# Optimization experiments

Measured on AMD Instinct MI355X. Metric: run time of the kernel, lower is better.

Reference implementation:

```python
import jax, jax.numpy as jnp
import numpy as np

N_ATOMS = 50000
N_PAIRS = 800000
X_DIM = 3
N_PROP = 64


def setup_inputs() -> dict:
    key = jax.random.key(0)
    k1, k2, k3, k4 = jax.random.split(key, 4)
    ind_2 = jax.random.randint(k1, (N_PAIRS, 2), 0, N_ATOMS, dtype=jnp.int64 if jax.config.jax_enable_x64 else jnp.int32)
    px = jax.random.normal(k2, (N_ATOMS, X_DIM, N_PROP), dtype=jnp.float32)
    wi = jax.random.normal(k3, (N_PROP, N_PROP), dtype=jnp.float32) / np.sqrt(N_PROP)
    wj = jax.random.normal(k4, (N_PROP, N_PROP), dtype=jnp.float32) / np.sqrt(N_PROP)
    return {"ind_2": ind_2, "px": px, "wi": wi, "wj": wj}


def reference(ind_2, px, wi, wj):
    # gather node equivariant props per edge endpoint
    px_i = px[ind_2[:, 0]]  # (n_pairs, x, n_prop)
    px_j = px[ind_2[:, 1]]  # (n_pairs, x, n_prop)
    # weighted branch: Dense(no bias) on last dim for each endpoint, then sum
    return jnp.einsum("pxz,zg->pxg", px_i, wi) + jnp.einsum("pxz,zg->pxg", px_j, wj)
```

## Files before the change

kernel.cpp:

```cpp
#include <hip/hip_runtime.h>

#define NPROP 64

typedef float vf4 __attribute__((ext_vector_type(4)));

__global__ __launch_bounds__(64, 2)
void transform_kernel(const float* __restrict__ px,
                      const float* __restrict__ wi,
                      const float* __restrict__ wj,
                      float* __restrict__ A,
                      float* __restrict__ B,
                      int nrows) {
    const int g = threadIdx.x;

    float WA[NPROP], WB[NPROP];
#pragma unroll
    for (int z = 0; z < NPROP; ++z) {
        WA[z] = wi[z * NPROP + g];
        WB[z] = wj[z * NPROP + g];
    }

    for (int r = blockIdx.x; r < nrows; r += gridDim.x) {
        const float* __restrict__ row = px + (size_t)r * NPROP;
        float a = 0.0f, b = 0.0f;
#pragma unroll
        for (int z = 0; z < NPROP; ++z) {
            float v = row[z];
            a = fmaf(v, WA[z], a);
            b = fmaf(v, WB[z], b);
        }
        A[(size_t)r * NPROP + g] = a;
        B[(size_t)r * NPROP + g] = b;
    }
}

__global__ __launch_bounds__(256)
void gather_add_kernel(const int* __restrict__ ind,
                       const vf4* __restrict__ A,
                       const vf4* __restrict__ B,
                       vf4* __restrict__ out,
                       int total_f4) {
    int f = blockIdx.x * 256 + threadIdx.x;
    if (f >= total_f4) return;
    unsigned uf = (unsigned)f;
    unsigned pair = uf / 48u;
    unsigned r = uf - pair * 48u;
    int i = ind[2u * pair];
    int j = ind[2u * pair + 1u];
    vf4 a = A[(size_t)i * 48u + r];
    vf4 b = B[(size_t)j * 48u + r];
    __builtin_nontemporal_store(a + b, out + f);
}

__global__ __launch_bounds__(256)
void naive_fused_kernel(const int* __restrict__ ind,
                        const float* __restrict__ px,
                        const float* __restrict__ wi,
                        const float* __restrict__ wj,
                        float* __restrict__ out,
                        int npairs) {
    __shared__ float swi[NPROP * NPROP];
    __shared__ float swj[NPROP * NPROP];
    for (int t = threadIdx.x; t < NPROP * NPROP; t += 256) {
        swi[t] = wi[t];
        swj[t] = wj[t];
    }
    __syncthreads();

    const int lane = threadIdx.x & 63;
    const int w = threadIdx.x >> 6;
    const long nrows = (long)npairs * 3;
    for (long row = (long)blockIdx.x * 4 + w; row < nrows;
         row += (long)gridDim.x * 4) {
        int p = (int)(row / 3);
        int x = (int)(row - (long)p * 3);
        int i = ind[2 * p];
        int j = ind[2 * p + 1];
        const float* ri = px + ((size_t)i * 3 + x) * NPROP;
        const float* rj = px + ((size_t)j * 3 + x) * NPROP;
        float acc = 0.0f;
        for (int z = 0; z < NPROP; ++z) {
            acc = fmaf(ri[z], swi[z * NPROP + lane],
                       fmaf(rj[z], swj[z * NPROP + lane], acc));
        }
        out[row * NPROP + lane] = acc;
    }
}

extern "C" void kernel_launch(void* const* d_in, const int* in_sizes, int n_in,
                              void* d_out, int out_size, void* d_ws, size_t ws_size,
                              hipStream_t stream) {
    const int* ind = (const int*)d_in[0];
    const float* px = (const float*)d_in[1];
    const float* wi = (const float*)d_in[2];
    const float* wj = (const float*)d_in[3];
    float* out = (float*)d_out;

    const int npairs = in_sizes[0] / 2;
    const int nrows = in_sizes[1] / NPROP;

    const size_t need = 2 * (size_t)nrows * NPROP * sizeof(float);
    if (ws_size >= need) {
        float* A = (float*)d_ws;
        float* B = A + (size_t)nrows * NPROP;
        transform_kernel<<<4096, 64, 0, stream>>>(px, wi, wj, A, B, nrows);
        int total_f4 = npairs * 48;
        gather_add_kernel<<<(total_f4 + 255) / 256, 256, 0, stream>>>(
            ind, (const vf4*)A, (const vf4*)B, (vf4*)out, total_f4);
    } else {
        naive_fused_kernel<<<8192, 256, 0, stream>>>(ind, px, wi, wj, out,
                                                     npairs);
    }
}
```

Measured before the change: 876.8 us.

## Fuse gather and matmul into one MFMA kernel with split-bf16 weights

Drops the two-pass approach, which precomputed transformed per-atom tables and then gathered them, in favour of a single fused kernel. Each wave gathers 16 edge rows of px for both endpoints and multiplies them against wi and wj stacked as a K=128 operand, using bf16 MFMA. Precision is kept close to fp32 by splitting operands into high and low bf16 parts and issuing three MFMAs per step. This removes the workspace write and reread, but the output is now written as scalar strided stores instead of vectorized ones, and px rows are re-gathered per edge.

```diff
diff --git a/kernel.cpp b/kernel.cpp
--- a/kernel.cpp
+++ b/kernel.cpp
@@ -2,88 +2,112 @@
 
 #define NPROP 64
 
-typedef float vf4 __attribute__((ext_vector_type(4)));
+typedef float f32x4 __attribute__((ext_vector_type(4)));
+typedef short bf16x8 __attribute__((ext_vector_type(8)));
 
-__global__ __launch_bounds__(64, 2)
-void transform_kernel(const float* __restrict__ px,
-                      const float* __restrict__ wi,
-                      const float* __restrict__ wj,
-                      float* __restrict__ A,
-                      float* __restrict__ B,
-                      int nrows) {
-    const int g = threadIdx.x;
+__device__ inline unsigned short f2bf(float f) {
+    unsigned u = __float_as_uint(f);
+    u += 0x7fffu + ((u >> 16) & 1u);
+    return (unsigned short)(u >> 16);
+}
+__device__ inline float bf2f(unsigned short h) {
+    return __uint_as_float(((unsigned)h) << 16);
+}
 
-    float WA[NPROP], WB[NPROP];
+__device__ inline void cvt8(float4 a, float4 b, bf16x8& hi, bf16x8& lo) {
+    float f[8] = {a.x, a.y, a.z, a.w, b.x, b.y, b.z, b.w};
 #pragma unroll
-    for (int z = 0; z < NPROP; ++z) {
-        WA[z] = wi[z * NPROP + g];
-        WB[z] = wj[z * NPROP + g];
-    }
-
-    for (int r = blockIdx.x; r < nrows; r += gridDim.x) {
-        const float* __restrict__ row = px + (size_t)r * NPROP;
-        float a = 0.0f, b = 0.0f;
-#pragma unroll
-        for (int z = 0; z < NPROP; ++z) {
-            float v = row[z];
-            a = fmaf(v, WA[z], a);
-            b = fmaf(v, WB[z], b);
-        }
-        A[(size_t)r * NPROP + g] = a;
-        B[(size_t)r * NPROP + g] = b;
+    for (int e = 0; e < 8; ++e) {
+        unsigned short h = f2bf(f[e]);
+        hi[e] = (short)h;
+        lo[e] = (short)f2bf(f[e] - bf2f(h));
     }
 }
 
 __global__ __launch_bounds__(256)
-void gather_add_kernel(const int* __restrict__ ind,
-                       const vf4* __restrict__ A,
-                       const vf4* __restrict__ B,
-                       vf4* __restrict__ out,
-                       int total_f4) {
-    int f = blockIdx.x * 256 + threadIdx.x;
-    if (f >= total_f4) return;
-    unsigned uf = (unsigned)f;
-    unsigned pair = uf / 48u;
-    unsigned r = uf - pair * 48u;
-    int i = ind[2u * pair];
-    int j = ind[2u * pair + 1u];
-    vf4 a = A[(size_t)i * 48u + r];
-    vf4 b = B[(size_t)j * 48u + r];
-    __builtin_nontemporal_store(a + b, out + f);
-}
+void fused_mfma_kernel(const int* __restrict__ ind,
+                       const float* __restrict__ px,
+                       const float* __restrict__ wi,
+                       const float* __restrict__ wj,
+                       float* __restrict__ out,
+                       int npairs) {
+    __shared__ short Bh[8192];
+    __shared__ short Bl[8192];
 
-__global__ __launch_bounds__(256)
-void naive_fused_kernel(const int* __restrict__ ind,
-                        const float* __restrict__ px,
-                        const float* __restrict__ wi,
-                        const float* __restrict__ wj,
-                        float* __restrict__ out,
-                        int npairs) {
-    __shared__ float swi[NPROP * NPROP];
-    __shared__ float swj[NPROP * NPROP];
-    for (int t = threadIdx.x; t < NPROP * NPROP; t += 256) {
-        swi[t] = wi[t];
-        swj[t] = wj[t];
+    for (int u = threadIdx.x; u < 2048; u += 256) {
+        int src = u & 1023;
+        const float4 v = ((const float4*)(u < 1024 ? wi : wj))[src];
+        int k  = (u < 1024 ? 0 : 64) + (src >> 4);
+        int g0 = (src & 15) * 4;
+        int sl  = k >> 5;
+        int hi3 = (k >> 3) & 3;
+        int e   = k & 7;
+        float fv[4] = {v.x, v.y, v.z, v.w};
+#pragma unroll
+        for (int c = 0; c < 4; ++c) {
+            int g = g0 + c;
+            int lane = hi3 * 16 + (g & 15);
+            int n = g >> 4;
+            int idx = (((sl * 4 + n) * 64 + lane) << 3) + e;
+            unsigned short h = f2bf(fv[c]);
+            Bh[idx] = (short)h;
+            Bl[idx] = (short)f2bf(fv[c] - bf2f(h));
+        }
     }
     __syncthreads();
 
-    const int lane = threadIdx.x & 63;
-    const int w = threadIdx.x >> 6;
-    const long nrows = (long)npairs * 3;
-    for (long row = (long)blockIdx.x * 4 + w; row < nrows;
-         row += (long)gridDim.x * 4) {
-        int p = (int)(row / 3);
-        int x = (int)(row - (long)p * 3);
-        int i = ind[2 * p];
-        int j = ind[2 * p + 1];
-        const float* ri = px + ((size_t)i * 3 + x) * NPROP;
-        const float* rj = px + ((size_t)j * 3 + x) * NPROP;
-        float acc = 0.0f;
-        for (int z = 0; z < NPROP; ++z) {
-            acc = fmaf(ri[z], swi[z * NPROP + lane],
-                       fmaf(rj[z], swj[z * NPROP + lane], acc));
+    const int l  = threadIdx.x & 63;
+    const int wv = threadIdx.x >> 6;
+    const long nrows  = (long)npairs * 3;
+    const int  ntiles = (int)((nrows + 15) >> 4);
+    const int  nwaves = gridDim.x * 4;
+
+    for (int t = blockIdx.x * 4 + wv; t < ntiles; t += nwaves) {
+        long row = (long)t * 16 + (l & 15);
+        if (row >= nrows) row = nrows - 1;
+        unsigned ur = (unsigned)row;
+        unsigned p  = ur / 3u;
+        unsigned x  = ur - p * 3u;
+        int i = ind[2u * p];
+        int j = ind[2u * p + 1u];
+        const float* pi = px + ((size_t)i * 3 + x) * NPROP;
+        const float* pj = px + ((size_t)j * 3 + x) * NPROP;
+        int c0 = (l >> 4) * 8;
+        float4 v0 = *(const float4*)(pi + c0);
+        float4 v1 = *(const float4*)(pi + c0 + 4);
+        float4 v2 = *(const float4*)(pi + 32 + c0);
+        float4 v3 = *(const float4*)(pi + 32 + c0 + 4);
+        float4 u0 = *(const float4*)(pj + c0);
+        float4 u1 = *(const float4*)(pj + c0 + 4);
+        float4 u2 = *(const float4*)(pj + 32 + c0);
+        float4 u3 = *(const float4*)(pj + 32 + c0 + 4);
+
+        bf16x8 Ah[4], Al[4];
+        cvt8(v0, v1, Ah[0], Al[0]);
+        cvt8(v2, v3, Ah[1], Al[1]);
+        cvt8(u0, u1, Ah[2], Al[2]);
+        cvt8(u2, u3, Ah[3], Al[3]);
+
+#pragma unroll
+        for (int n = 0; n < 4; ++n) {
+            f32x4 acc = {0.f, 0.f, 0.f, 0.f};
+#pragma unroll
+            for (int sl = 0; sl < 4; ++sl) {
+                int bidx = ((sl * 4 + n) * 64 + l) << 3;
+                bf16x8 bh = *(const bf16x8*)&Bh[bidx];
+                bf16x8 bl = *(const bf16x8*)&Bl[bidx];
+                acc = __builtin_amdgcn_mfma_f32_16x16x32_bf16(Ah[sl], bh, acc, 0, 0, 0);
+                acc = __builtin_amdgcn_mfma_f32_16x16x32_bf16(Al[sl], bh, acc, 0, 0, 0);
+                acc = __builtin_amdgcn_mfma_f32_16x16x32_bf16(Ah[sl], bl, acc, 0, 0, 0);
+            }
+#pragma unroll
+            for (int q = 0; q < 4; ++q) {
+                long grow = (long)t * 16 + (l >> 4) * 4 + q;
+                if (grow < nrows)
+                    __builtin_nontemporal_store(
+                        acc[q], out + grow * NPROP + n * 16 + (l & 15));
+            }
         }
-        out[row * NPROP + lane] = acc;
     }
 }
 
@@ -97,18 +121,6 @@
     float* out = (float*)d_out;
 
     const int npairs = in_sizes[0] / 2;
-    const int nrows = in_sizes[1] / NPROP;
 
-    const size_t need = 2 * (size_t)nrows * NPROP * sizeof(float);
-    if (ws_size >= need) {
-        float* A = (float*)d_ws;
-        float* B = A + (size_t)nrows * NPROP;
-        transform_kernel<<<4096, 64, 0, stream>>>(px, wi, wj, A, B, nrows);
-        int total_f4 = npairs * 48;
-        gather_add_kernel<<<(total_f4 + 255) / 256, 256, 0, stream>>>(
-            ind, (const vf4*)A, (const vf4*)B, (vf4*)out, total_f4);
-    } else {
-        naive_fused_kernel<<<8192, 256, 0, stream>>>(ind, px, wi, wj, out,
-                                                     npairs);
-    }
+    fused_mfma_kernel<<<2048, 256, 0, stream>>>(ind, px, wi, wj, out, npairs);
 }
```

Result: faster. 816.2 us (-6.9%).
